# Kernel optimization log

Measured on AMD Instinct MI355X. Metric: run time of the kernel, lower is better.

## Reference

```python
import jax, jax.numpy as jnp
import numpy as np

B, S, D = 512, 512, 256
N_TARGETS, N_HEADS, COND_DIM = 8, 4, 64
Q = N_TARGETS * N_HEADS
NEG_INF = -1e9


def _alibi_slopes(n_heads):
    return jnp.array([2.0 ** (-8.0 * (h + 1) / n_heads) for h in range(n_heads)], dtype=jnp.float32)


def setup_inputs() -> dict:
    key = jax.random.key(0)
    ks = jax.random.split(key, 9)
    keys = jax.random.normal(ks[0], (B, S, D), dtype=jnp.float32)
    # variable-length histories: real games at positions 0..n_real-1 (oldest first)
    lengths = jax.random.randint(ks[1], (B, 1), 1, S + 1)
    mask = jnp.arange(S)[None, :] < lengths  # [B, S] bool
    context = jax.random.normal(ks[2], (B, COND_DIM), dtype=jnp.float32)
    queries = 0.02 * jax.random.normal(ks[3], (N_TARGETS, N_HEADS, D), dtype=jnp.float32)
    key_w = jax.random.normal(ks[4], (D, D), dtype=jnp.float32) / np.sqrt(D)
    value_w = jax.random.normal(ks[5], (D, D), dtype=jnp.float32) / np.sqrt(D)
    log_temperature = 0.1 * jax.random.normal(ks[6], (N_TARGETS,), dtype=jnp.float32)
    # cond_proj is zero-initialised in the original; use small random for a non-trivial path
    cond_w = 0.01 * jax.random.normal(ks[7], (Q * D, COND_DIM), dtype=jnp.float32)
    cond_b = 0.01 * jax.random.normal(ks[8], (Q * D,), dtype=jnp.float32)
    return {"keys": keys, "mask": mask, "context": context, "queries": queries,
            "key_w": key_w, "value_w": value_w, "log_temperature": log_temperature,
            "cond_w": cond_w, "cond_b": cond_b}


def reference(keys, mask, context, queries, key_w, value_w, log_temperature, cond_w, cond_b):
    scale = D ** (-0.5)
    k = jnp.einsum('bsd,ed->bse', keys, key_w)    # key_proj (no bias)
    v = jnp.einsum('bsd,ed->bse', keys, value_w)  # value_proj (no bias)
    q_flat = queries.reshape(Q, D)
    delta = (context @ cond_w.T + cond_b).reshape(-1, Q, D)  # [B, Q, D]
    q_per_row = q_flat[None] + delta
    attn = jnp.einsum('bqd,bsd->bqs', q_per_row, k) * scale  # [B, Q, S]
    # per-target learned temperature, repeat_interleave over heads
    inv_t = jnp.repeat(jnp.exp(-log_temperature), N_HEADS).reshape(1, Q, 1)
    attn = attn * inv_t
    # ALiBi time-decay bias
    n_real = mask.sum(axis=-1, keepdims=True)                 # [B, 1]
    positions = jnp.arange(S)
    games_ago = jnp.clip(n_real - 1 - positions[None, :], 0).astype(jnp.float32)  # [B, S]
    slopes = jnp.tile(_alibi_slopes(N_HEADS), N_TARGETS).reshape(1, Q, 1)
    attn = attn - slopes * games_ago[:, None, :]
    attn = jnp.where(mask[:, None, :], attn, NEG_INF)
    attn = jax.nn.softmax(attn, axis=-1)
    out = jnp.einsum('bqs,bsd->bqd', attn, v)                 # [B, Q, D]
    return out.reshape(-1, N_TARGETS, N_HEADS * D)


if __name__ == "__main__":
    out = reference(**setup_inputs())
    print(out.shape)
```

## Files before the change

kernel.cpp:

```cpp
#include <hip/hip_runtime.h>

typedef short bf16x8_t __attribute__((ext_vector_type(8)));
typedef float f32x4_t  __attribute__((ext_vector_type(4)));

#define MFMA16(a,b,c) __builtin_amdgcn_mfma_f32_16x16x32_bf16(a,b,c,0,0,0)

__device__ __forceinline__ unsigned short f2b(float x){
  unsigned u = __float_as_uint(x);
  u += 0x7fffu + ((u >> 16) & 1u);
  return (unsigned short)(u >> 16);
}

__device__ __forceinline__ void bar_lgkm(){
  asm volatile("s_waitcnt lgkmcnt(0)" ::: "memory");
  __builtin_amdgcn_s_barrier();
  __builtin_amdgcn_sched_barrier(0);
}

__global__ __launch_bounds__(256) void setup_qs(
    const float* __restrict__ context, const float* __restrict__ queries,
    const float* __restrict__ logt, const float* __restrict__ condw,
    const float* __restrict__ condb,
    const float* __restrict__ kw, const float* __restrict__ vw,
    const int* __restrict__ mask,
    unsigned short* __restrict__ qs,
    unsigned short* __restrict__ wktb, unsigned short* __restrict__ wvb,
    int* __restrict__ nreal){
  int bid = blockIdx.x, tid = threadIdx.x;
  if (bid < 2048){
    __shared__ float ctx_l[8 * 64];
    int q   = bid & 31;
    int b0  = (bid >> 5) * 8;
    int qd  = q * 256 + tid;
    float4 cw[16];
    #pragma unroll
    for (int j = 0; j < 16; ++j) cw[j] = *(const float4*)(condw + (size_t)qd * 64 + 4 * j);
    float qbias = queries[qd] + condb[qd];
    float sc = 0.0625f * __expf(-logt[q >> 2]);
    ctx_l[tid]       = context[(size_t)b0 * 64 + tid];
    ctx_l[tid + 256] = context[(size_t)b0 * 64 + tid + 256];
    __syncthreads();
    #pragma unroll
    for (int b = 0; b < 8; ++b){
      const float4* cl = (const float4*)(ctx_l + b * 64);
      float acc = 0.f;
      #pragma unroll
      for (int j = 0; j < 16; ++j){
        float4 cv = cl[j]; float4 w4 = cw[j];
        acc += cv.x * w4.x + cv.y * w4.y + cv.z * w4.z + cv.w * w4.w;
      }
      qs[((size_t)(b0 + b) * 32 + q) * 256 + tid] = f2b((qbias + acc) * sc);
    }
  } else if (bid < 2304){
    int i = (bid - 2048) * 256 + tid;
    int d = i >> 8, e = i & 255;
    wktb[i] = f2b(kw[e * 256 + d]);
    wvb[i]  = f2b(vw[i]);
  } else {
    int b = (bid - 2304) * 4 + (tid >> 6), l = tid & 63;
    int s_ = 0;
    #pragma unroll
    for (int j = 0; j < 8; ++j) s_ += mask[(size_t)b * 512 + j * 64 + l];
    #pragma unroll
    for (int k = 1; k < 64; k <<= 1) s_ += __shfl_xor(s_, k);
    if (l == 0) nreal[b] = s_ < 1 ? 1 : (s_ > 512 ? 512 : s_);
  }
}

__global__ __launch_bounds__(256, 2) void attn_part(
    const float* __restrict__ keys, const int* __restrict__ nreal,
    const unsigned short* __restrict__ qs, const unsigned short* __restrict__ wkt,
    const unsigned short* __restrict__ wvb, float* __restrict__ out){
  __shared__ unsigned short K[64 * 256];
  __shared__ unsigned short vT[256 * 64];
  __shared__ unsigned short Pl[32 * 64];
  __shared__ float denl[32];

  int b = (blockIdx.x & 7) * 64 + (blockIdx.x >> 3);
  int n_real = nreal[b];

  int tid = threadIdx.x, w = tid >> 6, l = tid & 63, h = l >> 4, c = l & 15;
  int qg = w & 1, rp = w >> 1;
  if (tid < 32) denl[tid] = 0.f;

  f32x4_t zero4 = {0.f, 0.f, 0.f, 0.f};

  bf16x8_t bIe, bIo;
  #pragma unroll
  for (int j = 0; j < 8; ++j){
    bIe[j] = (h == (c >> 3)     && j == (c & 7)) ? (short)0x3F80 : (short)0;
    bIo[j] = (h == 2 + (c >> 3) && j == (c & 7)) ? (short)0x3F80 : (short)0;
  }

  const float* kptr = keys + ((size_t)b * 512 + w) * 256 + 4 * l;
  float4 R[16];
  #pragma unroll
  for (int j = 0; j < 16; ++j) R[j] = *(const float4*)(kptr + j * 1024);

  bf16x8_t qf[8];
  {
    unsigned short* qtmp = vT;
    f32x4_t qa[4][2];
    #pragma unroll
    for (int mt = 0; mt < 4; ++mt){ qa[mt][0] = zero4; qa[mt][1] = zero4; }
    #pragma unroll
    for (int kk = 0; kk < 8; ++kk){
      int colk = kk * 32 + 8 * h;
      bf16x8_t B0 = *(const bf16x8_t*)(qs + ((size_t)b * 32 + c) * 256 + colk);
      bf16x8_t B1 = *(const bf16x8_t*)(qs + ((size_t)b * 32 + 16 + c) * 256 + colk);
      #pragma unroll
      for (int mt = 0; mt < 4; ++mt){
        int d = 64 * w + 16 * mt + c;
        bf16x8_t Av = *(const bf16x8_t*)(wkt + (size_t)d * 256 + colk);
        qa[mt][0] = MFMA16(Av, B0, qa[mt][0]);
        qa[mt][1] = MFMA16(Av, B1, qa[mt][1]);
      }
    }
    #pragma unroll
    for (int mt = 0; mt < 4; ++mt)
      #pragma unroll
      for (int qt2 = 0; qt2 < 2; ++qt2)
        #pragma unroll
        for (int i = 0; i < 4; ++i){
          int q = 16 * qt2 + c;
          int d = 64 * w + 16 * mt + 4 * h + i;
          qtmp[q * 256 + (d ^ ((q & 7) << 3))] = f2b(qa[mt][qt2][i]);
        }
    bar_lgkm();
    #pragma unroll
    for (int kk = 0; kk < 8; ++kk){
      int q = 16 * qg + c;
      qf[kk] = *(const bf16x8_t*)&qtmp[q * 256 + ((kk * 32 + 8 * h) ^ ((q & 7) << 3))];
    }
  }

  float slope0 = exp2f(-2.0f * (float)((c & 3) + 1));

  f32x4_t ao[2][4];
  #pragma unroll
  for (int q2 = 0; q2 < 2; ++q2)
    #pragma unroll
    for (int nt = 0; nt < 4; ++nt) ao[q2][nt] = zero4;

  int tend = (n_real + 63) >> 6;

  for (int it = 0; it < tend; ++it){
    int s0 = it * 64;
    const float* knext = kptr + (size_t)(it + 1) * (64 * 256);
    #pragma unroll
    for (int j = 0; j < 16; ++j){
      int row = 4 * j + w;
      int d4 = 4 * l;
      float4 kv = R[j];
      if (it + 1 < tend) R[j] = *(const float4*)(knext + j * 1024);
      uint2 p;
      p.x = (unsigned)f2b(kv.x) | ((unsigned)f2b(kv.y) << 16);
      p.y = (unsigned)f2b(kv.z) | ((unsigned)f2b(kv.w) << 16);
      *(uint2*)&K[row * 256 + (d4 ^ ((row & 7) << 3))] = p;
    }
    bar_lgkm();

    f32x4_t as_[2];
    as_[0] = zero4; as_[1] = zero4;
    #pragma unroll
    for (int kk = 0; kk < 8; ++kk){
      int colk = kk * 32 + 8 * h;
      {
        int r0_ = 16 * (2 * rp) + c, r1_ = 16 * (2 * rp + 1) + c;
        bf16x8_t A0 = *(const bf16x8_t*)&K[r0_ * 256 + (colk ^ ((r0_ & 7) << 3))];
        bf16x8_t A1 = *(const bf16x8_t*)&K[r1_ * 256 + (colk ^ ((r1_ & 7) << 3))];
        as_[0] = MFMA16(A0, qf[kk], as_[0]);
        as_[1] = MFMA16(A1, qf[kk], as_[1]);
      }
      if ((kk >> 1) == w){
        int ntb = (kk & 1) << 1;
        int e0 = 64 * w + 16 * ntb + c;
        int e1 = e0 + 16;
        #pragma unroll
        for (int g = 0; g < 4; ++g){
          int rg_ = 16 * g + c;
          bf16x8_t Ag = *(const bf16x8_t*)&K[rg_ * 256 + (colk ^ ((rg_ & 7) << 3))];
          f32x4_t tE = MFMA16(Ag, bIe, zero4);
          f32x4_t tO = MFMA16(Ag, bIo, zero4);
          int t0 = 16 * g + 4 * h;
          uint2 p;
          p.x = (unsigned)f2b(tE[0]) | ((unsigned)f2b(tE[1]) << 16);
          p.y = (unsigned)f2b(tE[2]) | ((unsigned)f2b(tE[3]) << 16);
          *(uint2*)&vT[e0 * 64 + (t0 ^ ((e0 & 7) << 3))] = p;
          p.x = (unsigned)f2b(tO[0]) | ((unsigned)f2b(tO[1]) << 16);
          p.y = (unsigned)f2b(tO[2]) | ((unsigned)f2b(tO[3]) << 16);
          *(uint2*)&vT[e1 * 64 + (t0 ^ ((e1 & 7) << 3))] = p;
        }
      }
    }

    {
      float qs_ = 0.f;
      int q = 16 * qg + c;
      #pragma unroll
      for (int g2 = 0; g2 < 2; ++g2){
        int gr = 2 * rp + g2;
        float e_[4];
        #pragma unroll
        for (int i = 0; i < 4; ++i){
          int s = s0 + 16 * gr + 4 * h + i;
          float ga = (float)(n_real - 1 - s);
          bool valid = (s < n_real);
          float v = valid ? __expf(as_[g2][i] - slope0 * ga) : 0.f;
          e_[i] = v; qs_ += v;
        }
        int t0 = 16 * gr + 4 * h;
        uint2 p;
        p.x = (unsigned)f2b(e_[0]) | ((unsigned)f2b(e_[1]) << 16);
        p.y = (unsigned)f2b(e_[2]) | ((unsigned)f2b(e_[3]) << 16);
        *(uint2*)&Pl[q * 64 + (t0 ^ ((q & 7) << 3))] = p;
      }
      float r = qs_ + __shfl_xor(qs_, 16); r += __shfl_xor(r, 32);
      if (l < 16) atomicAdd(&denl[q], r);
    }
    bar_lgkm();

    #pragma unroll
    for (int ts = 0; ts < 2; ++ts){
      int t0 = 32 * ts + 8 * h;
      bf16x8_t Ap0 = *(const bf16x8_t*)&Pl[c * 64 + (t0 ^ ((c & 7) << 3))];
      bf16x8_t Ap1 = *(const bf16x8_t*)&Pl[(16 + c) * 64 + (t0 ^ (((16 + c) & 7) << 3))];
      #pragma unroll
      for (int nt = 0; nt < 4; ++nt){
        int e = 64 * w + 16 * nt + c;
        bf16x8_t Bv = *(const bf16x8_t*)&vT[e * 64 + (t0 ^ ((e & 7) << 3))];
        ao[0][nt] = MFMA16(Ap0, Bv, ao[0][nt]);
        ao[1][nt] = MFMA16(Ap1, Bv, ao[1][nt]);
      }
    }
  }

  {
    unsigned short* at = K;
    #pragma unroll
    for (int q2 = 0; q2 < 2; ++q2)
      #pragma unroll
      for (int i = 0; i < 4; ++i){
        int q = 16 * q2 + 4 * h + i;
        float invd = 1.f / denl[q];
        #pragma unroll
        for (int nt = 0; nt < 4; ++nt){
          int e = 64 * w + 16 * nt + c;
          at[q * 256 + (e ^ ((q & 7) << 3))] = f2b(ao[q2][nt][i] * invd);
        }
      }
    __syncthreads();

    f32x4_t a2[2][4];
    #pragma unroll
    for (int m = 0; m < 2; ++m)
      #pragma unroll
      for (int nt = 0; nt < 4; ++nt) a2[m][nt] = zero4;
    #pragma unroll
    for (int kk = 0; kk < 8; ++kk){
      bf16x8_t A[2];
      #pragma unroll
      for (int m = 0; m < 2; ++m){
        int row = c + 16 * m;
        A[m] = *(const bf16x8_t*)&at[row * 256 + ((kk * 32 + 8 * h) ^ ((row & 7) << 3))];
      }
      #pragma unroll
      for (int nt = 0; nt < 4; ++nt){
        int ep = 64 * w + 16 * nt + c;
        bf16x8_t Bv = *(const bf16x8_t*)(wvb + (size_t)ep * 256 + kk * 32 + 8 * h);
        #pragma unroll
        for (int m = 0; m < 2; ++m) a2[m][nt] = MFMA16(A[m], Bv, a2[m][nt]);
      }
    }
    #pragma unroll
    for (int m = 0; m < 2; ++m)
      #pragma unroll
      for (int nt = 0; nt < 4; ++nt)
        #pragma unroll
        for (int i = 0; i < 4; ++i){
          int row = 16 * m + 4 * h + i;
          int ep = 64 * w + 16 * nt + c;
          out[((size_t)b * 32 + row) * 256 + ep] = a2[m][nt][i];
        }
  }
}

extern "C" void kernel_launch(void* const* d_in, const int* in_sizes, int n_in,
                              void* d_out, int out_size, void* d_ws, size_t ws_size,
                              hipStream_t stream){
  const float* keys    = (const float*)d_in[0];
  const int*   mask    = (const int*)d_in[1];
  const float* context = (const float*)d_in[2];
  const float* queries = (const float*)d_in[3];
  const float* key_w   = (const float*)d_in[4];
  const float* value_w = (const float*)d_in[5];
  const float* logt    = (const float*)d_in[6];
  const float* cond_w  = (const float*)d_in[7];
  const float* cond_b  = (const float*)d_in[8];
  float* out = (float*)d_out;

  unsigned short* wkt = (unsigned short*)d_ws;
  unsigned short* wvb = wkt + 65536;
  unsigned short* qs  = wvb + 65536;
  int*   nreal = (int*)(qs + (size_t)16384 * 256);

  hipLaunchKernelGGL(setup_qs, dim3(2432), dim3(256), 0, stream,
                     context, queries, logt, cond_w, cond_b, key_w, value_w, mask,
                     qs, wkt, wvb, nreal);
  hipLaunchKernelGGL(attn_part, dim3(512), dim3(256), 0, stream, keys, nreal, qs, wkt, wvb, out);
}
```

Before: 81.55 us.

## Split attention over two sequence halves with atomic last-block merge

Each batch row's keys are split into two 256-position chunks handled by separate blocks, doubling the grid to 1024. Blocks whose chunk lies past n_real exit early. When both chunks are active, partial accumulators and denominators go to global workspace, and the last block to arrive (found with an atomic counter) merges them before the value projection. The aim is to balance load across the variable history lengths and use more CUs. The cost is extra global traffic and fences for long rows. The merge adds no max-subtraction, which is consistent with the un-normalised accumulation the kernel already uses.

```diff
diff --git a/kernel.cpp b/kernel.cpp
--- a/kernel.cpp
+++ b/kernel.cpp
@@ -25,7 +25,7 @@
     const int* __restrict__ mask,
     unsigned short* __restrict__ qs,
     unsigned short* __restrict__ wktb, unsigned short* __restrict__ wvb,
-    int* __restrict__ nreal){
+    int* __restrict__ nreal, int* __restrict__ cnt){
   int bid = blockIdx.x, tid = threadIdx.x;
   if (bid < 2048){
     __shared__ float ctx_l[8 * 64];
@@ -56,7 +56,7 @@
     int d = i >> 8, e = i & 255;
     wktb[i] = f2b(kw[e * 256 + d]);
     wvb[i]  = f2b(vw[i]);
-  } else {
+  } else if (bid < 2432){
     int b = (bid - 2304) * 4 + (tid >> 6), l = tid & 63;
     int s_ = 0;
     #pragma unroll
@@ -64,20 +64,29 @@
     #pragma unroll
     for (int k = 1; k < 64; k <<= 1) s_ += __shfl_xor(s_, k);
     if (l == 0) nreal[b] = s_ < 1 ? 1 : (s_ > 512 ? 512 : s_);
+  } else {
+    cnt[tid] = 0; cnt[tid + 256] = 0;
   }
 }
 
 __global__ __launch_bounds__(256, 2) void attn_part(
     const float* __restrict__ keys, const int* __restrict__ nreal,
     const unsigned short* __restrict__ qs, const unsigned short* __restrict__ wkt,
-    const unsigned short* __restrict__ wvb, float* __restrict__ out){
+    const unsigned short* __restrict__ wvb,
+    float* __restrict__ accw, float* __restrict__ dengw, int* __restrict__ cnt,
+    float* __restrict__ out){
   __shared__ unsigned short K[64 * 256];
   __shared__ unsigned short vT[256 * 64];
   __shared__ unsigned short Pl[32 * 64];
   __shared__ float denl[32];
-
-  int b = (blockIdx.x & 7) * 64 + (blockIdx.x >> 3);
+  __shared__ int flag;
+
+  int lbid = (blockIdx.x & 7) * 128 + (blockIdx.x >> 3);
+  int b = lbid >> 1, ch = lbid & 1;
   int n_real = nreal[b];
+  int sbase = ch * 256;
+  if (sbase >= n_real) return;
+  bool solo = (n_real <= 256);
 
   int tid = threadIdx.x, w = tid >> 6, l = tid & 63, h = l >> 4, c = l & 15;
   int qg = w & 1, rp = w >> 1;
@@ -92,7 +101,10 @@
     bIo[j] = (h == 2 + (c >> 3) && j == (c & 7)) ? (short)0x3F80 : (short)0;
   }
 
-  const float* kptr = keys + ((size_t)b * 512 + w) * 256 + 4 * l;
+  int tv = n_real - sbase;
+  int tend = (tv + 63) >> 6; if (tend > 4) tend = 4;
+
+  const float* kptr = keys + ((size_t)b * 512 + sbase + w) * 256 + 4 * l;
   float4 R[16];
   #pragma unroll
   for (int j = 0; j < 16; ++j) R[j] = *(const float4*)(kptr + j * 1024);
@@ -142,10 +154,8 @@
     #pragma unroll
     for (int nt = 0; nt < 4; ++nt) ao[q2][nt] = zero4;
 
-  int tend = (n_real + 63) >> 6;
-
   for (int it = 0; it < tend; ++it){
-    int s0 = it * 64;
+    int s0 = sbase + it * 64;
     const float* knext = kptr + (size_t)(it + 1) * (64 * 256);
     #pragma unroll
     for (int j = 0; j < 16; ++j){
@@ -235,8 +245,8 @@
     }
   }
 
-  {
-    unsigned short* at = K;
+  float nv[2][4][4];
+  if (solo){
     #pragma unroll
     for (int q2 = 0; q2 < 2; ++q2)
       #pragma unroll
@@ -244,9 +254,69 @@
         int q = 16 * q2 + 4 * h + i;
         float invd = 1.f / denl[q];
         #pragma unroll
+        for (int nt = 0; nt < 4; ++nt) nv[q2][nt][i] = ao[q2][nt][i] * invd;
+      }
+  } else {
+    float* mya = accw + ((size_t)(ch * 512 + b) * 32) * 256;
+    #pragma unroll
+    for (int q2 = 0; q2 < 2; ++q2)
+      #pragma unroll
+      for (int nt = 0; nt < 4; ++nt){
+        int e = 64 * w + 16 * nt + c;
+        #pragma unroll
+        for (int i = 0; i < 4; ++i){
+          int q = 16 * q2 + 4 * h + i;
+          __hip_atomic_store(&mya[q * 256 + e], ao[q2][nt][i],
+                             __ATOMIC_RELAXED, __HIP_MEMORY_SCOPE_AGENT);
+        }
+      }
+    if (tid < 32)
+      __hip_atomic_store(&dengw[(ch * 512 + b) * 32 + tid], denl[tid],
+                         __ATOMIC_RELAXED, __HIP_MEMORY_SCOPE_AGENT);
+    __syncthreads();
+    if (tid == 0){
+      __threadfence();
+      flag = __hip_atomic_fetch_add(&cnt[b], 1, __ATOMIC_ACQ_REL, __HIP_MEMORY_SCOPE_AGENT);
+    }
+    __syncthreads();
+    if (flag == 0) return;
+    __threadfence();
+    if (tid < 32){
+      float d0 = __hip_atomic_load(&dengw[b * 32 + tid], __ATOMIC_RELAXED, __HIP_MEMORY_SCOPE_AGENT);
+      float d1 = __hip_atomic_load(&dengw[(512 + b) * 32 + tid], __ATOMIC_RELAXED, __HIP_MEMORY_SCOPE_AGENT);
+      denl[tid] = d0 + d1;
+    }
+    __syncthreads();
+    const float* a0p = accw + ((size_t)b * 32) * 256;
+    const float* a1p = accw + ((size_t)(512 + b) * 32) * 256;
+    #pragma unroll
+    for (int q2 = 0; q2 < 2; ++q2)
+      #pragma unroll
+      for (int i = 0; i < 4; ++i){
+        int q = 16 * q2 + 4 * h + i;
+        float invd = 1.f / denl[q];
+        #pragma unroll
         for (int nt = 0; nt < 4; ++nt){
           int e = 64 * w + 16 * nt + c;
-          at[q * 256 + (e ^ ((q & 7) << 3))] = f2b(ao[q2][nt][i] * invd);
+          float v0 = __hip_atomic_load(&a0p[q * 256 + e], __ATOMIC_RELAXED, __HIP_MEMORY_SCOPE_AGENT);
+          float v1 = __hip_atomic_load(&a1p[q * 256 + e], __ATOMIC_RELAXED, __HIP_MEMORY_SCOPE_AGENT);
+          nv[q2][nt][i] = (v0 + v1) * invd;
+        }
+      }
+  }
+
+  {
+    unsigned short* at = K;
+    __syncthreads();
+    #pragma unroll
+    for (int q2 = 0; q2 < 2; ++q2)
+      #pragma unroll
+      for (int i = 0; i < 4; ++i){
+        int q = 16 * q2 + 4 * h + i;
+        #pragma unroll
+        for (int nt = 0; nt < 4; ++nt){
+          int e = 64 * w + 16 * nt + c;
+          at[q * 256 + (e ^ ((q & 7) << 3))] = f2b(nv[q2][nt][i]);
         }
       }
     __syncthreads();
@@ -302,10 +372,14 @@
   unsigned short* wkt = (unsigned short*)d_ws;
   unsigned short* wvb = wkt + 65536;
   unsigned short* qs  = wvb + 65536;
-  int*   nreal = (int*)(qs + (size_t)16384 * 256);
-
-  hipLaunchKernelGGL(setup_qs, dim3(2432), dim3(256), 0, stream,
+  float* accw  = (float*)(qs + (size_t)16384 * 256);
+  float* dengw = accw + (size_t)2 * 512 * 32 * 256;
+  int*   cnt   = (int*)(dengw + 2 * 512 * 32);
+  int*   nreal = cnt + 512;
+
+  hipLaunchKernelGGL(setup_qs, dim3(2433), dim3(256), 0, stream,
                      context, queries, logt, cond_w, cond_b, key_w, value_w, mask,
-                     qs, wkt, wvb, nreal);
-  hipLaunchKernelGGL(attn_part, dim3(512), dim3(256), 0, stream, keys, nreal, qs, wkt, wvb, out);
-}
+                     qs, wkt, wvb, nreal, cnt);
+  hipLaunchKernelGGL(attn_part, dim3(1024), dim3(256), 0, stream,
+                     keys, nreal, qs, wkt, wvb, accw, dengw, cnt, out);
+}
```

Measured after the change: 159.7 us. 1.96x slower.
